# Kernel tuning notes

Hardware: AMD Instinct MI355X
Metric: run time of the kernel (lower is better)

The kernel has to match this reference:

```python
import jax, jax.numpy as jnp
import numpy as np

B, N, H, HEADS = 8, 1024, 512, 4  # batch graphs, nodes/graph, graph_hsz, attention heads
R = 64  # relations per graph (passthrough)


def setup_inputs() -> dict:
    key = jax.random.key(0)
    k1, k2, k3, k4, k5, k6, k7 = jax.random.split(key, 7)
    adjs = jax.random.randint(k1, (B, N, N), 0, 2, dtype=jnp.int32)  # 0 => masked
    nodes = jax.random.normal(k2, (B, N, H), dtype=jnp.float32)
    triples = jax.random.normal(k3, (B, R, H), dtype=jnp.float32)   # unused in gat path
    relations = jax.random.normal(k4, (B, R, H), dtype=jnp.float32)  # passthrough
    node_num = jnp.full((B,), N, dtype=jnp.int32)  # all graphs full => no padding branch
    s = 1.0 / np.sqrt(H)
    Wq = (jax.random.normal(k5, (H, H), dtype=jnp.float32) * s)
    Wk = (jax.random.normal(k6, (H, H), dtype=jnp.float32) * s)
    Wv = (jax.random.normal(k7, (H, H), dtype=jnp.float32) * s)
    return {"adjs": adjs, "triples": triples, "nodes": nodes, "node_num": node_num,
            "relations": relations, "Wq": Wq, "Wk": Wk, "Wv": Wv}


def reference(adjs, triples, nodes, node_num, relations, Wq, Wk, Wv):
    b, n, h = nodes.shape
    dk = h // HEADS
    scale = 1.0 / jnp.sqrt(jnp.float32(h))  # torch divides by sqrt(key_dim)=sqrt(H)

    def to_heads(x, W):  # [B,N,H] -> [B,heads,N,dk]; matches split(dim=-1)+stack
        return (x @ W).reshape(b, n, HEADS, dk).transpose(0, 2, 1, 3)

    Q = to_heads(nodes, Wq)
    K = to_heads(nodes, Wk)
    V = to_heads(nodes, Wv)
    att = jnp.einsum('bhnd,bhmd->bhnm', Q, K) * scale
    att = jnp.where((adjs == 0)[:, None, :, :], -jnp.inf, att)
    p = jax.nn.softmax(att, axis=-1)  # dropout_p = blockdrop = 0.0 => identity
    out = jnp.einsum('bhnm,bhmd->bhnd', p, V)
    out = out.transpose(0, 2, 1, 3).reshape(b, n, h)  # concat heads along feature dim
    out = jax.nn.relu(out)
    return (out, relations)
```

## Files before the change

### kernel.cpp

```cpp
#include <hip/hip_runtime.h>
#include <stdint.h>

typedef __attribute__((ext_vector_type(4))) float f32x4;
typedef __attribute__((ext_vector_type(16))) float f32x16;
typedef __attribute__((ext_vector_type(8))) short bf16x8;
typedef unsigned long long ull;

#define GLB_AS const __attribute__((address_space(1)))
#define LDS_AS __attribute__((address_space(3)))

__device__ __forceinline__ short f2bf(float f) {
    union { float f; unsigned u; } x; x.f = f;
    unsigned r = x.u + 0x7FFFu + ((x.u >> 16) & 1u);
    return (short)(r >> 16);
}

__global__ void k_pre(const float* __restrict__ nodes, short* __restrict__ nodes_bf,
                      const float* __restrict__ Wq, const float* __restrict__ Wk,
                      const float* __restrict__ Wv, short* __restrict__ WT,
                      const int* __restrict__ adjs, unsigned* __restrict__ packed) {
    int bi = blockIdx.x, tid = threadIdx.x;
    if (bi < 2048) {
        int i = (bi * 256 + tid) * 8;
        float4 a = *(const float4*)(nodes + i);
        float4 b = *(const float4*)(nodes + i + 4);
        bf16x8 v;
        v[0] = f2bf(a.x); v[1] = f2bf(a.y); v[2] = f2bf(a.z); v[3] = f2bf(a.w);
        v[4] = f2bf(b.x); v[5] = f2bf(b.y); v[6] = f2bf(b.z); v[7] = f2bf(b.w);
        *(bf16x8*)(nodes_bf + i) = v;
    } else if (bi < 5120) {
        int g = (bi - 2048) * 256 + tid;
        int j = g >> 9, k = g & 511;
        int w = j >> 9, n = j & 511;
        const float* W = (w == 0) ? Wq : (w == 1) ? Wk : Wv;
        WT[g] = f2bf(W[k * 512 + n]);
    } else {
        int g = (bi - 5120) * 256 + tid;
        int wv = g >> 6, lane = g & 63;
        ull m = __ballot(adjs[(size_t)wv * 64 + lane] != 0);
        if (lane == 0) *(ull*)(packed + (size_t)wv * 2) = m;
    }
}

__global__ __launch_bounds__(256) void k_gemm_qkv(const short* __restrict__ A,
                                                  const short* __restrict__ WT,
                                                  short* __restrict__ C) {
    __shared__ short Asm[2][128 * 32];
    __shared__ short Bsm[2][128 * 32];
    const int tid = threadIdx.x;
    const int l = tid & 63, w = tid >> 6;
    const int wr = w >> 1, wc = w & 1;
    const int c16 = l & 15, g = l >> 4;
    const int wg = blockIdx.x;
    const int swz = (wg & 7) * 96 + (wg >> 3);
    const int row0 = (swz / 12) * 128, n0 = (swz % 12) * 128;
    f32x4 acc[4][4] = {};

    auto stage = [&](int kt, int bsel) {
        const int k0 = kt * 32;
#pragma unroll
        for (int i = 0; i < 2; ++i) {
            int ch = tid + 256 * i;
            int r = ch >> 2, gc = ch & 3;
            __builtin_amdgcn_global_load_lds((GLB_AS unsigned*)(A + (row0 + r) * 512 + k0 + 8 * gc),
                                             (LDS_AS unsigned*)(&Asm[bsel][ch * 8]), 16, 0, 0);
            __builtin_amdgcn_global_load_lds((GLB_AS unsigned*)(WT + (n0 + r) * 512 + k0 + 8 * gc),
                                             (LDS_AS unsigned*)(&Bsm[bsel][ch * 8]), 16, 0, 0);
        }
    };

    stage(0, 0);
    asm volatile("s_waitcnt vmcnt(0)" ::: "memory");
    __syncthreads();

    for (int kt = 0; kt < 16; ++kt) {
        const int cur = kt & 1;
        if (kt < 15) stage(kt + 1, cur ^ 1);
        bf16x8 af[4], bfr[4];
#pragma unroll
        for (int mf = 0; mf < 4; ++mf)
            af[mf] = *(const bf16x8*)&Asm[cur][(wr * 64 + mf * 16 + c16) * 32 + 8 * g];
#pragma unroll
        for (int nf = 0; nf < 4; ++nf)
            bfr[nf] = *(const bf16x8*)&Bsm[cur][(wc * 64 + nf * 16 + c16) * 32 + 8 * g];
#pragma unroll
        for (int mf = 0; mf < 4; ++mf)
#pragma unroll
            for (int nf = 0; nf < 4; ++nf)
                acc[mf][nf] = __builtin_amdgcn_mfma_f32_16x16x32_bf16(af[mf], bfr[nf], acc[mf][nf], 0, 0, 0);
        asm volatile("s_waitcnt vmcnt(0)" ::: "memory");
        __syncthreads();
    }
#pragma unroll
    for (int mf = 0; mf < 4; ++mf)
#pragma unroll
        for (int nf = 0; nf < 4; ++nf) {
            const float cs = (n0 + wc * 64 + nf * 16 < 512) ? 0.06375872022286384f : 1.0f;
#pragma unroll
            for (int r = 0; r < 4; ++r) {
                int row = row0 + wr * 64 + mf * 16 + 4 * g + r;
                int col = n0 + wc * 64 + nf * 16 + c16;
                C[row * 1536 + col] = f2bf(acc[mf][nf][r] * cs);
            }
        }
}

__global__ __launch_bounds__(256) void k_mid(const short* __restrict__ QKV, short* __restrict__ Vt2,
                                             const float* __restrict__ rel_in, float* __restrict__ rel_out) {
    __shared__ short tile[64 * 65];
    const int bi = blockIdx.x, t = threadIdx.x;
    if (bi >= 1024) {
        int i = ((bi - 1024) * 256 + t) * 4;
        *(float4*)(rel_out + i) = *(const float4*)(rel_in + i);
        return;
    }
    const int b = bi >> 7, n0 = ((bi >> 3) & 15) * 64, d0 = (bi & 7) * 64;
#pragma unroll
    for (int i = 0; i < 16; ++i) {
        int idx = t + 256 * i;
        int nn = idx >> 6, dd = idx & 63;
        tile[nn * 65 + dd] = QKV[(b * 1024 + n0 + nn) * 1536 + 1024 + d0 + dd];
    }
    __syncthreads();
#pragma unroll
    for (int i = 0; i < 2; ++i) {
        int c = t + 256 * i;
        int dd = c >> 3, nl = (c & 7) * 8;
        int dg = d0 + dd;
        int h = dg >> 7, dh = dg & 127;
        bf16x8 v;
#pragma unroll
        for (int e = 0; e < 8; ++e)
            v[e] = tile[(nl + e) * 65 + dd];
        *(bf16x8*)(Vt2 + ((((size_t)(b * 4 + h)) * 128 + ((n0 + nl) >> 3)) * 128 + dh) * 8) = v;
    }
}

__global__ __launch_bounds__(512, 1) void k_attn(const short* __restrict__ QKV, const short* __restrict__ Vt2,
                                                 const unsigned* __restrict__ packed, float* __restrict__ out) {
    __shared__ char smem[66560];
    short* Ksm = (short*)smem;
    float* Osh = (float*)smem;
    float* lsh = (float*)(smem + 65536);
    const int bh = blockIdx.x;
    const int b = bh >> 2, h = bh & 3;
    const int q0 = blockIdx.y * 128;
    const int tid = threadIdx.x, l = tid & 63, wid = tid >> 6;
    const int mg = wid >> 2, wq = wid & 3;
    const int gt = tid & 255;
    const int l31 = l & 31, hi = l >> 5;
    const int qw = q0 + wq * 32;

    bf16x8 aq[8];
    const short* Qb = QKV + (size_t)(b * 1024 + qw + l31) * 1536 + h * 128;
#pragma unroll
    for (int kk = 0; kk < 8; ++kk)
        aq[kk] = *(const bf16x8*)(Qb + kk * 16 + hi * 8);

    f32x16 acc[4] = {};
    float l_lane = 0.f;

    const short* Kbase = QKV + (size_t)(b * 1024) * 1536 + 512 + h * 128;
    const short* V2b = Vt2 + (size_t)(b * 4 + h) * 131072;
    const ull* adjq = (const ull*)packed + (size_t)(b * 1024 + qw + l31) * 16 + mg * 8;

    auto stageK = [&](int t, int bsel) {
        const int m0 = mg * 512 + t * 64;
        short* dst = Ksm + (mg * 2 + bsel) * 8192;
#pragma unroll
        for (int i = 0; i < 4; ++i) {
            int ch = gt + 256 * i;
            int mr = ch >> 4, gc = ch & 15;
            int gs = gc ^ (mr & 15);
            __builtin_amdgcn_global_load_lds((GLB_AS unsigned*)(Kbase + (size_t)(m0 + mr) * 1536 + 8 * gs),
                                             (LDS_AS unsigned*)(dst + ch * 8), 16, 0, 0);
        }
    };

    ull mcur = adjq[0], mnxt = 0;
    stageK(0, 0);
    asm volatile("s_waitcnt vmcnt(0)" ::: "memory");
    __builtin_amdgcn_s_barrier();

    for (int t = 0; t < 8; ++t) {
        const int cur = t & 1;
        if (t < 7) {
            stageK(t + 1, cur ^ 1);
            mnxt = adjq[t + 1];
        }
        const int mc0 = mg * 64 + t * 8;
        bf16x8 bv[2][4];
#pragma unroll
        for (int ks = 0; ks < 2; ++ks)
#pragma unroll
            for (int dd = 0; dd < 4; ++dd)
                bv[ks][dd] = *(const bf16x8*)(V2b + (((size_t)(mc0 + 2 * ks + hi)) * 128 + dd * 32 + l31) * 8);

        const short* Kb = Ksm + (mg * 2 + cur) * 8192;
        f32x16 s[2];
        s[0] = (f32x16)0.f; s[1] = (f32x16)0.f;
        __builtin_amdgcn_s_setprio(1);
#pragma unroll
        for (int kk = 0; kk < 8; ++kk)
#pragma unroll
            for (int mm = 0; mm < 2; ++mm) {
                const int row = mm * 32 + l31;
                const int chunk = (2 * kk + hi) ^ (row & 15);
                bf16x8 ak = *(const bf16x8*)&Kb[row * 128 + chunk * 8];
                s[mm] = __builtin_amdgcn_mfma_f32_32x32x16_bf16(ak, aq[kk], s[mm], 0, 0, 0);
            }
        __builtin_amdgcn_s_setprio(0);

        unsigned pk[2][4][2];
        float lt = 0.f;
#pragma unroll
        for (int mm = 0; mm < 2; ++mm) {
            const unsigned mshift = (unsigned)(mcur >> (32 * mm + 4 * hi));
#pragma unroll
            for (int j = 0; j < 4; ++j) {
                float p[4];
#pragma unroll
                for (int r = 0; r < 4; ++r) {
                    float e = __builtin_amdgcn_exp2f(s[mm][4 * j + r]);
                    p[r] = ((mshift >> (8 * j + r)) & 1u) ? e : 0.f;
                }
                lt += (p[0] + p[1]) + (p[2] + p[3]);
                asm("v_cvt_pk_bf16_f32 %0, %1, %2" : "=v"(pk[mm][j][0]) : "v"(p[0]), "v"(p[1]));
                asm("v_cvt_pk_bf16_f32 %0, %1, %2" : "=v"(pk[mm][j][1]) : "v"(p[2]), "v"(p[3]));
            }
        }
        l_lane += lt;

        union fragu { unsigned u[4]; bf16x8 v; };
#pragma unroll
        for (int mm = 0; mm < 2; ++mm) {
            fragu frag[2];
#pragma unroll
            for (int kh = 0; kh < 2; ++kh) {
                unsigned a0 = pk[mm][2 * kh][0], a1 = pk[mm][2 * kh][1];
                unsigned b0 = pk[mm][2 * kh + 1][0], b1 = pk[mm][2 * kh + 1][1];
                unsigned rx0 = (unsigned)__shfl_xor((int)a0, 32);
                unsigned rx1 = (unsigned)__shfl_xor((int)a1, 32);
                unsigned rx2 = (unsigned)__shfl_xor((int)b0, 32);
                unsigned rx3 = (unsigned)__shfl_xor((int)b1, 32);
                fragu f;
                f.u[0] = hi ? rx2 : a0;
                f.u[1] = hi ? rx3 : a1;
                f.u[2] = hi ? b0 : rx0;
                f.u[3] = hi ? b1 : rx1;
                frag[kh] = f;
            }
            __builtin_amdgcn_s_setprio(1);
#pragma unroll
            for (int kh = 0; kh < 2; ++kh) {
                const int ksl = 2 * mm + kh;
#pragma unroll
                for (int dd = 0; dd < 4; ++dd) {
                    bf16x8 bvv;
                    if (ksl < 2) bvv = bv[ksl][dd];
                    else         bvv = *(const bf16x8*)(V2b + (((size_t)(mc0 + 2 * ksl + hi)) * 128 + dd * 32 + l31) * 8);
                    acc[dd] = __builtin_amdgcn_mfma_f32_32x32x16_bf16(frag[kh].v, bvv, acc[dd], 0, 0, 0);
                }
            }
            __builtin_amdgcn_s_setprio(0);
        }

        mcur = mnxt;
        asm volatile("s_waitcnt vmcnt(0)" ::: "memory");
        __builtin_amdgcn_s_barrier();
    }

    l_lane += __shfl_xor(l_lane, 32);
    if (hi == 0) lsh[mg * 128 + wq * 32 + l31] = l_lane;

    if (mg == 1) {
#pragma unroll
        for (int dd = 0; dd < 4; ++dd)
#pragma unroll
            for (int j = 0; j < 4; ++j)
#pragma unroll
                for (int r = 0; r < 4; ++r) {
                    int qrow = wq * 32 + r + 8 * j + 4 * hi;
                    Osh[qrow * 128 + dd * 32 + l31] = acc[dd][4 * j + r];
                }
    }
    __syncthreads();
    if (mg == 0) {
        float inv[4][2];
#pragma unroll
        for (int j = 0; j < 4; ++j)
#pragma unroll
            for (int r2 = 0; r2 < 2; ++r2) {
                inv[j][r2] = 0.f;
            }
        float invq[16];
#pragma unroll
        for (int j = 0; j < 4; ++j)
#pragma unroll
            for (int r = 0; r < 4; ++r) {
                int qrow = wq * 32 + r + 8 * j + 4 * hi;
                invq[4 * j + r] = 1.f / (lsh[qrow] + lsh[128 + qrow]);
            }
#pragma unroll
        for (int dd = 0; dd < 4; ++dd)
#pragma unroll
            for (int j = 0; j < 4; ++j)
#pragma unroll
                for (int r = 0; r < 4; ++r) {
                    int qrow = wq * 32 + r + 8 * j + 4 * hi;
                    float o = (acc[dd][4 * j + r] + Osh[qrow * 128 + dd * 32 + l31]) * invq[4 * j + r];
                    out[(size_t)(b * 1024 + q0 + qrow) * 512 + h * 128 + dd * 32 + l31] = fmaxf(o, 0.f);
                }
    }
}

extern "C" void kernel_launch(void* const* d_in, const int* in_sizes, int n_in,
                              void* d_out, int out_size, void* d_ws, size_t ws_size,
                              hipStream_t stream) {
    const int*   adjs      = (const int*)d_in[0];
    const float* nodes     = (const float*)d_in[2];
    const float* relations = (const float*)d_in[4];
    const float* Wq        = (const float*)d_in[5];
    const float* Wk        = (const float*)d_in[6];
    const float* Wv        = (const float*)d_in[7];

    char* ws = (char*)d_ws;
    short* nodes_bf   = (short*)(ws);
    short* WT         = (short*)(ws + 8388608);
    short* QKV        = (short*)(ws + 9961472);
    short* Vt2        = (short*)(ws + 35127296);
    unsigned* adjpack = (unsigned*)(ws + 43515904);

    float* out     = (float*)d_out;
    float* out_rel = out + 4194304;

    k_pre<<<dim3(37888), dim3(256), 0, stream>>>(nodes, nodes_bf, Wq, Wk, Wv, WT, adjs, adjpack);
    k_gemm_qkv<<<dim3(768), dim3(256), 0, stream>>>(nodes_bf, WT, QKV);
    k_mid<<<dim3(1280), dim3(256), 0, stream>>>(QKV, Vt2, relations, out_rel);
    k_attn<<<dim3(32, 8), dim3(512), 0, stream>>>(QKV, Vt2, adjpack, out);
}
```

Baseline: 82.15 us.

## Pre-swizzle K into MFMA fragment layout and load it directly into registers

Adds a K transpose pass in k_mid that writes K in a per-head, MFMA-fragment-ordered layout. The attention kernel then drops LDS staging and barriers and loads K fragments straight from global memory into registers, prefetching one tile ahead over 16 smaller steps. Launch bounds are raised to allow two blocks per CU. The trade-off is an extra K copy pass plus more register pressure, and K is now read from global/L2 by every wave instead of being shared through LDS.

```diff
diff --git a/kernel.cpp b/kernel.cpp
--- a/kernel.cpp
+++ b/kernel.cpp
@@ -106,14 +106,23 @@
 }
 
 __global__ __launch_bounds__(256) void k_mid(const short* __restrict__ QKV, short* __restrict__ Vt2,
+                                             short* __restrict__ Kt2,
                                              const float* __restrict__ rel_in, float* __restrict__ rel_out) {
-    __shared__ short tile[64 * 65];
     const int bi = blockIdx.x, t = threadIdx.x;
+    if (bi >= 1280) {
+        int g = (bi - 1280) * 256 + t;
+        int c = g & 63, m = (g >> 6) & 1023, b = g >> 16;
+        int h = c >> 4, khc = c & 15;
+        bf16x8 v = *(const bf16x8*)(QKV + (size_t)(b * 1024 + m) * 1536 + 512 + c * 8);
+        *(bf16x8*)(Kt2 + ((((size_t)(b * 4 + h) * 32 + (m >> 5)) * 16 + khc) * 32 + (m & 31)) * 8) = v;
+        return;
+    }
     if (bi >= 1024) {
         int i = ((bi - 1024) * 256 + t) * 4;
         *(float4*)(rel_out + i) = *(const float4*)(rel_in + i);
         return;
     }
+    __shared__ short tile[64 * 65];
     const int b = bi >> 7, n0 = ((bi >> 3) & 15) * 64, d0 = (bi & 7) * 64;
 #pragma unroll
     for (int i = 0; i < 16; ++i) {
@@ -136,10 +145,10 @@
     }
 }
 
-__global__ __launch_bounds__(512, 1) void k_attn(const short* __restrict__ QKV, const short* __restrict__ Vt2,
+__global__ __launch_bounds__(512, 2) void k_attn(const short* __restrict__ QKV, const short* __restrict__ Kt2,
+                                                 const short* __restrict__ Vt2,
                                                  const unsigned* __restrict__ packed, float* __restrict__ out) {
     __shared__ char smem[66560];
-    short* Ksm = (short*)smem;
     float* Osh = (float*)smem;
     float* lsh = (float*)(smem + 65536);
     const int bh = blockIdx.x;
@@ -147,7 +156,6 @@
     const int q0 = blockIdx.y * 128;
     const int tid = threadIdx.x, l = tid & 63, wid = tid >> 6;
     const int mg = wid >> 2, wq = wid & 3;
-    const int gt = tid & 255;
     const int l31 = l & 31, hi = l >> 5;
     const int qw = q0 + wq * 32;
 
@@ -160,114 +168,89 @@
     f32x16 acc[4] = {};
     float l_lane = 0.f;
 
-    const short* Kbase = QKV + (size_t)(b * 1024) * 1536 + 512 + h * 128;
+    const short* K2b = Kt2 + (size_t)(b * 4 + h) * 131072;
     const short* V2b = Vt2 + (size_t)(b * 4 + h) * 131072;
-    const ull* adjq = (const ull*)packed + (size_t)(b * 1024 + qw + l31) * 16 + mg * 8;
-
-    auto stageK = [&](int t, int bsel) {
-        const int m0 = mg * 512 + t * 64;
-        short* dst = Ksm + (mg * 2 + bsel) * 8192;
-#pragma unroll
-        for (int i = 0; i < 4; ++i) {
-            int ch = gt + 256 * i;
-            int mr = ch >> 4, gc = ch & 15;
-            int gs = gc ^ (mr & 15);
-            __builtin_amdgcn_global_load_lds((GLB_AS unsigned*)(Kbase + (size_t)(m0 + mr) * 1536 + 8 * gs),
-                                             (LDS_AS unsigned*)(dst + ch * 8), 16, 0, 0);
-        }
-    };
-
-    ull mcur = adjq[0], mnxt = 0;
-    stageK(0, 0);
-    asm volatile("s_waitcnt vmcnt(0)" ::: "memory");
-    __builtin_amdgcn_s_barrier();
-
-    for (int t = 0; t < 8; ++t) {
-        const int cur = t & 1;
-        if (t < 7) {
-            stageK(t + 1, cur ^ 1);
-            mnxt = adjq[t + 1];
-        }
-        const int mc0 = mg * 64 + t * 8;
-        bf16x8 bv[2][4];
+    const unsigned* adjw = packed + (size_t)(b * 1024 + qw + l31) * 32 + mg * 16;
+
+    bf16x8 kcur[8], knxt[8], vcur[8];
+    {
+        const int mt = mg * 16;
+#pragma unroll
+        for (int kk = 0; kk < 8; ++kk)
+            kcur[kk] = *(const bf16x8*)(K2b + ((size_t)(mt * 16 + 2 * kk + hi) * 32 + l31) * 8);
+    }
+    unsigned mcur = adjw[0];
+
+#pragma unroll
+    for (int t = 0; t < 16; ++t) {
+        const int mc0 = mg * 64 + t * 4;
 #pragma unroll
         for (int ks = 0; ks < 2; ++ks)
 #pragma unroll
             for (int dd = 0; dd < 4; ++dd)
-                bv[ks][dd] = *(const bf16x8*)(V2b + (((size_t)(mc0 + 2 * ks + hi)) * 128 + dd * 32 + l31) * 8);
-
-        const short* Kb = Ksm + (mg * 2 + cur) * 8192;
-        f32x16 s[2];
-        s[0] = (f32x16)0.f; s[1] = (f32x16)0.f;
+                vcur[ks * 4 + dd] = *(const bf16x8*)(V2b + ((size_t)(mc0 + 2 * ks + hi) * 128 + dd * 32 + l31) * 8);
+        unsigned mnx = 0;
+        if (t < 15) {
+            const int mt = mg * 16 + t + 1;
+#pragma unroll
+            for (int kk = 0; kk < 8; ++kk)
+                knxt[kk] = *(const bf16x8*)(K2b + ((size_t)(mt * 16 + 2 * kk + hi) * 32 + l31) * 8);
+            mnx = adjw[t + 1];
+        }
+
+        f32x16 s = (f32x16)0.f;
         __builtin_amdgcn_s_setprio(1);
 #pragma unroll
         for (int kk = 0; kk < 8; ++kk)
-#pragma unroll
-            for (int mm = 0; mm < 2; ++mm) {
-                const int row = mm * 32 + l31;
-                const int chunk = (2 * kk + hi) ^ (row & 15);
-                bf16x8 ak = *(const bf16x8*)&Kb[row * 128 + chunk * 8];
-                s[mm] = __builtin_amdgcn_mfma_f32_32x32x16_bf16(ak, aq[kk], s[mm], 0, 0, 0);
+            s = __builtin_amdgcn_mfma_f32_32x32x16_bf16(kcur[kk], aq[kk], s, 0, 0, 0);
+        __builtin_amdgcn_s_setprio(0);
+
+        unsigned pk[4][2];
+        const unsigned mshift = mcur >> (4 * hi);
+        float lt = 0.f;
+#pragma unroll
+        for (int j = 0; j < 4; ++j) {
+            float p[4];
+#pragma unroll
+            for (int r = 0; r < 4; ++r) {
+                float e = __builtin_amdgcn_exp2f(s[4 * j + r]);
+                p[r] = ((mshift >> (8 * j + r)) & 1u) ? e : 0.f;
             }
+            lt += (p[0] + p[1]) + (p[2] + p[3]);
+            asm("v_cvt_pk_bf16_f32 %0, %1, %2" : "=v"(pk[j][0]) : "v"(p[0]), "v"(p[1]));
+            asm("v_cvt_pk_bf16_f32 %0, %1, %2" : "=v"(pk[j][1]) : "v"(p[2]), "v"(p[3]));
+        }
+        l_lane += lt;
+
+        union fragu { unsigned u[4]; bf16x8 v; };
+        fragu frag[2];
+#pragma unroll
+        for (int kh = 0; kh < 2; ++kh) {
+            unsigned a0 = pk[2 * kh][0], a1 = pk[2 * kh][1];
+            unsigned b0 = pk[2 * kh + 1][0], b1 = pk[2 * kh + 1][1];
+            unsigned rx0 = (unsigned)__shfl_xor((int)a0, 32);
+            unsigned rx1 = (unsigned)__shfl_xor((int)a1, 32);
+            unsigned rx2 = (unsigned)__shfl_xor((int)b0, 32);
+            unsigned rx3 = (unsigned)__shfl_xor((int)b1, 32);
+            fragu f;
+            f.u[0] = hi ? rx2 : a0;
+            f.u[1] = hi ? rx3 : a1;
+            f.u[2] = hi ? b0 : rx0;
+            f.u[3] = hi ? b1 : rx1;
+            frag[kh] = f;
+        }
+
+        __builtin_amdgcn_s_setprio(1);
+#pragma unroll
+        for (int ks = 0; ks < 2; ++ks)
+#pragma unroll
+            for (int dd = 0; dd < 4; ++dd)
+                acc[dd] = __builtin_amdgcn_mfma_f32_32x32x16_bf16(frag[ks].v, vcur[ks * 4 + dd], acc[dd], 0, 0, 0);
         __builtin_amdgcn_s_setprio(0);
 
-        unsigned pk[2][4][2];
-        float lt = 0.f;
-#pragma unroll
-        for (int mm = 0; mm < 2; ++mm) {
-            const unsigned mshift = (unsigned)(mcur >> (32 * mm + 4 * hi));
-#pragma unroll
-            for (int j = 0; j < 4; ++j) {
-                float p[4];
-#pragma unroll
-                for (int r = 0; r < 4; ++r) {
-                    float e = __builtin_amdgcn_exp2f(s[mm][4 * j + r]);
-                    p[r] = ((mshift >> (8 * j + r)) & 1u) ? e : 0.f;
-                }
-                lt += (p[0] + p[1]) + (p[2] + p[3]);
-                asm("v_cvt_pk_bf16_f32 %0, %1, %2" : "=v"(pk[mm][j][0]) : "v"(p[0]), "v"(p[1]));
-                asm("v_cvt_pk_bf16_f32 %0, %1, %2" : "=v"(pk[mm][j][1]) : "v"(p[2]), "v"(p[3]));
-            }
-        }
-        l_lane += lt;
-
-        union fragu { unsigned u[4]; bf16x8 v; };
-#pragma unroll
-        for (int mm = 0; mm < 2; ++mm) {
-            fragu frag[2];
-#pragma unroll
-            for (int kh = 0; kh < 2; ++kh) {
-                unsigned a0 = pk[mm][2 * kh][0], a1 = pk[mm][2 * kh][1];
-                unsigned b0 = pk[mm][2 * kh + 1][0], b1 = pk[mm][2 * kh + 1][1];
-                unsigned rx0 = (unsigned)__shfl_xor((int)a0, 32);
-                unsigned rx1 = (unsigned)__shfl_xor((int)a1, 32);
-                unsigned rx2 = (unsigned)__shfl_xor((int)b0, 32);
-                unsigned rx3 = (unsigned)__shfl_xor((int)b1, 32);
-                fragu f;
-                f.u[0] = hi ? rx2 : a0;
-                f.u[1] = hi ? rx3 : a1;
-                f.u[2] = hi ? b0 : rx0;
-                f.u[3] = hi ? b1 : rx1;
-                frag[kh] = f;
-            }
-            __builtin_amdgcn_s_setprio(1);
-#pragma unroll
-            for (int kh = 0; kh < 2; ++kh) {
-                const int ksl = 2 * mm + kh;
-#pragma unroll
-                for (int dd = 0; dd < 4; ++dd) {
-                    bf16x8 bvv;
-                    if (ksl < 2) bvv = bv[ksl][dd];
-                    else         bvv = *(const bf16x8*)(V2b + (((size_t)(mc0 + 2 * ksl + hi)) * 128 + dd * 32 + l31) * 8);
-                    acc[dd] = __builtin_amdgcn_mfma_f32_32x32x16_bf16(frag[kh].v, bvv, acc[dd], 0, 0, 0);
-                }
-            }
-            __builtin_amdgcn_s_setprio(0);
-        }
-
-        mcur = mnxt;
-        asm volatile("s_waitcnt vmcnt(0)" ::: "memory");
-        __builtin_amdgcn_s_barrier();
+#pragma unroll
+        for (int kk = 0; kk < 8; ++kk) kcur[kk] = knxt[kk];
+        mcur = mnx;
     }
 
     l_lane += __shfl_xor(l_lane, 32);
@@ -286,13 +269,6 @@
     }
     __syncthreads();
     if (mg == 0) {
-        float inv[4][2];
-#pragma unroll
-        for (int j = 0; j < 4; ++j)
-#pragma unroll
-            for (int r2 = 0; r2 < 2; ++r2) {
-                inv[j][r2] = 0.f;
-            }
         float invq[16];
 #pragma unroll
         for (int j = 0; j < 4; ++j)
@@ -330,12 +306,13 @@
     short* QKV        = (short*)(ws + 9961472);
     short* Vt2        = (short*)(ws + 35127296);
     unsigned* adjpack = (unsigned*)(ws + 43515904);
+    short* Kt2        = (short*)(ws + 44564480);
 
     float* out     = (float*)d_out;
     float* out_rel = out + 4194304;
 
     k_pre<<<dim3(37888), dim3(256), 0, stream>>>(nodes, nodes_bf, Wq, Wk, Wv, WT, adjs, adjpack);
     k_gemm_qkv<<<dim3(768), dim3(256), 0, stream>>>(nodes_bf, WT, QKV);
-    k_mid<<<dim3(1280), dim3(256), 0, stream>>>(QKV, Vt2, relations, out_rel);
-    k_attn<<<dim3(32, 8), dim3(512), 0, stream>>>(QKV, Vt2, adjpack, out);
-}
+    k_mid<<<dim3(3328), dim3(256), 0, stream>>>(QKV, Vt2, Kt2, relations, out_rel);
+    k_attn<<<dim3(32, 8), dim3(512), 0, stream>>>(QKV, Kt2, Vt2, adjpack, out);
+}
```

Result: faster. 80.03 us (-2.6%).
